# Kernel optimization log

Hardware: AMD Instinct MI355X
Metric: run time of the kernel (lower is better)

## Reference

```python
import jax, jax.numpy as jnp
from jax import lax
import numpy as np

B = 65536


def setup_inputs() -> dict:
    key = jax.random.key(0)
    ks = jax.random.split(key, 7)
    return {
        "x": jax.random.normal(ks[0], (B, 1, 28, 28), dtype=jnp.float32),
        "W1": jax.random.normal(ks[1], (8, 1, 3, 3), dtype=jnp.float32) * 0.3,
        "b1": jax.random.normal(ks[2], (8,), dtype=jnp.float32) * 0.1,
        "W2": jax.random.normal(ks[3], (16, 8, 3, 3), dtype=jnp.float32) * 0.1,
        "b2": jax.random.normal(ks[4], (16,), dtype=jnp.float32) * 0.1,
        "Wfc": jax.random.normal(ks[5], (1, 784), dtype=jnp.float32) * 0.03,
        "bfc": jax.random.normal(ks[6], (1,), dtype=jnp.float32) * 0.1,
    }


def _conv(x, w, b):
    # NCHW / OIHW, stride 2, padding 1 (matches nn.Conv2d(kernel=3, stride=2, padding=1))
    y = lax.conv_general_dilated(x, w, window_strides=(2, 2), padding=((1, 1), (1, 1)))
    return y + b[None, :, None, None]


def reference(x, W1, b1, W2, b2, Wfc, bfc):
    z = jax.nn.relu(_conv(x, W1, b1))            # [B,8,14,14]
    z = jax.nn.relu(_conv(z, W2, b2))            # [B,16,7,7]
    z = z.reshape(z.shape[0], -1)                # [B,784], channel-major like torch flatten
    rates = jax.nn.softplus(z @ Wfc.T + bfc) + 0.001   # [B,1]
    rates = rates[:, 0]                          # [B]
    # Logistic ODE du/dt = -k*u, u(0)=1 over t in [0,1] -> u(1) = exp(-k)
    probs = 1.0 - jnp.exp(-rates)
    return jnp.clip(probs, 1e-6, 1.0 - 1e-6)
```

## Files before the change

### kernel.cpp

```cpp
#include <hip/hip_runtime.h>
#include <math.h>


typedef short bf16x8 __attribute__((ext_vector_type(8)));
typedef float f32x4  __attribute__((ext_vector_type(4)));

#define NBLOCKS 4096
#define Z1_RS 19
#define Z1_SLOTS (15 * Z1_RS)

static __device__ __forceinline__ short f2bf(float f) {
    union { float f; unsigned u; } v; v.f = f;
    unsigned r = v.u + 0x7FFF + ((v.u >> 16) & 1);
    return (short)(r >> 16);
}

__global__ __launch_bounds__(256, 4) void fused_cnn_mfma(
    const float* __restrict__ x,
    const float* __restrict__ W1, const float* __restrict__ b1,
    const float* __restrict__ W2, const float* __restrict__ b2,
    const float* __restrict__ Wfc, const float* __restrict__ bfc,
    float* __restrict__ out, int nimg)
{
    __shared__ float  simg[4][30 * 31];
    __shared__ bf16x8 sz1[4][Z1_SLOTS];

    const int tid  = threadIdx.x;
    const int w    = tid >> 6;
    const int lane = tid & 63;
    const int hi   = lane >> 4;
    const int lo   = lane & 15;

    for (int i = tid; i < 4 * 30 * 31; i += 256) ((float*)simg)[i] = 0.f;
    {
        bf16x8 zz = {0,0,0,0,0,0,0,0};
        for (int i = tid; i < 4 * Z1_SLOTS; i += 256) ((bf16x8*)sz1)[i] = zz;
    }

    bf16x8 wb[3];
    #pragma unroll
    for (int kk = 0; kk < 3; kk++) {
        const int tap = kk * 4 + hi;
        #pragma unroll
        for (int j = 0; j < 8; j++)
            wb[kk][j] = (tap < 9) ? f2bf(W2[lo * 72 + j * 9 + tap])
                                  : (short)0;
    }

    int posoff[4];
    #pragma unroll
    for (int t = 0; t < 4; t++) {
        int p = t * 16 + lo; if (p > 48) p = 48;
        int qy = p / 7, qx = p - qy * 7;
        posoff[t] = ((2 * qy) * Z1_RS + 2 * qx) * 16;
    }
    int tapoff[3];
    #pragma unroll
    for (int kk = 0; kk < 3; kk++) {
        int tap = kk * 4 + hi;
        int ty = tap / 3, tx = tap - ty * 3;
        tapoff[kk] = (tap < 9) ? (ty * Z1_RS + tx) * 16 : 0;
    }

    const float b2v = b2[lo];
    float wfc[4][4];
    #pragma unroll
    for (int t = 0; t < 4; t++)
        #pragma unroll
        for (int r = 0; r < 4; r++) {
            int p = t * 16 + hi * 4 + r;
            wfc[t][r] = (p < 49) ? Wfc[lo * 49 + p] : 0.f;
        }
    const float bfc0 = bfc[0];

    const int nquad = (nimg + 3) >> 2;
    const char* __restrict__ zb = (const char*)&sz1[w][0];

    for (int q = blockIdx.x; q < nquad; q += gridDim.x) {
        __syncthreads();

        {
            const float4* src = (const float4*)(x + (size_t)q * (4 * 784));
            for (int f = tid; f < 784; f += 256) {
                int im = f / 196, p4 = f - im * 196;
                if (q * 4 + im < nimg) {
                    float4 v = src[f];
                    int yy = p4 / 7, xx = (p4 - yy * 7) * 4;
                    float* d = &simg[im][(yy + 1) * 31 + xx + 1];
                    d[0] = v.x; d[1] = v.y; d[2] = v.z; d[3] = v.w;
                }
            }
        }
        __syncthreads();

        #pragma unroll
        for (int i = 0; i < 4; i++) {
            int p = i * 64 + lane;
            bool valid = (p < 196);
            int pc = valid ? p : 195;
            int py = pc / 14, px = pc - py * 14;
            const float* wbse = &simg[w][(2 * py) * 31 + 2 * px];
            float t0 = wbse[0],  t1 = wbse[1],  t2 = wbse[2];
            float t3 = wbse[31], t4 = wbse[32], t5 = wbse[33];
            float t6 = wbse[62], t7 = wbse[63], t8 = wbse[64];
            asm volatile("" : "+v"(t0), "+v"(t1), "+v"(t2), "+v"(t3), "+v"(t4),
                              "+v"(t5), "+v"(t6), "+v"(t7), "+v"(t8));
            bf16x8 zr;
            #pragma unroll
            for (int c = 0; c < 8; c += 2) {
                const float* wa = &W1[c * 9];
                const float* wc = &W1[(c + 1) * 9];
                float za = b1[c], zc = b1[c + 1];
                za = fmaf(t0, wa[0], za); zc = fmaf(t0, wc[0], zc);
                za = fmaf(t1, wa[1], za); zc = fmaf(t1, wc[1], zc);
                za = fmaf(t2, wa[2], za); zc = fmaf(t2, wc[2], zc);
                za = fmaf(t3, wa[3], za); zc = fmaf(t3, wc[3], zc);
                za = fmaf(t4, wa[4], za); zc = fmaf(t4, wc[4], zc);
                za = fmaf(t5, wa[5], za); zc = fmaf(t5, wc[5], zc);
                za = fmaf(t6, wa[6], za); zc = fmaf(t6, wc[6], zc);
                za = fmaf(t7, wa[7], za); zc = fmaf(t7, wc[7], zc);
                za = fmaf(t8, wa[8], za); zc = fmaf(t8, wc[8], zc);
                za = fmaxf(za, 0.f);      zc = fmaxf(zc, 0.f);
                zr[c]     = f2bf(za);
                zr[c + 1] = f2bf(zc);
            }
            if (valid) sz1[w][(py + 1) * Z1_RS + (px + 1)] = zr;
        }

        f32x4 acc[4];
        {
            f32x4 z4 = {0.f, 0.f, 0.f, 0.f};
            #pragma unroll
            for (int t = 0; t < 4; t++) acc[t] = z4;
        }
        #pragma unroll
        for (int t = 0; t < 4; t++) {
            #pragma unroll
            for (int kk = 0; kk < 3; kk++) {
                bf16x8 af = *(const bf16x8*)(zb + posoff[t] + tapoff[kk]);
                acc[t] = __builtin_amdgcn_mfma_f32_16x16x32_bf16(
                             af, wb[kk], acc[t], 0, 0, 0);
            }
        }

        float fc = 0.f;
        #pragma unroll
        for (int t = 0; t < 4; t++)
            #pragma unroll
            for (int r = 0; r < 4; r++) {
                float z = fmaxf(acc[t][r] + b2v, 0.f);
                fc = fmaf(z, wfc[t][r], fc);
            }
        #pragma unroll
        for (int off = 32; off > 0; off >>= 1)
            fc += __shfl_down(fc, off, 64);

        if (lane == 0) {
            int img = q * 4 + w;
            if (img < nimg) {
                float v    = fc + bfc0;
                float sp   = fmaxf(v, 0.f) + log1pf(expf(-fabsf(v)));
                float rate = sp + 0.001f;
                float pr   = 1.f - expf(-rate);
                out[img] = fminf(fmaxf(pr, 1e-6f), 1.f - 1e-6f);
            }
        }
    }
}

extern "C" void kernel_launch(void* const* d_in, const int* in_sizes, int n_in,
                              void* d_out, int out_size, void* d_ws, size_t ws_size,
                              hipStream_t stream) {
    const float* x   = (const float*)d_in[0];
    const float* W1  = (const float*)d_in[1];
    const float* b1  = (const float*)d_in[2];
    const float* W2  = (const float*)d_in[3];
    const float* b2  = (const float*)d_in[4];
    const float* Wfc = (const float*)d_in[5];
    const float* bfc = (const float*)d_in[6];
    float* out = (float*)d_out;

    const int nimg  = in_sizes[0] / 784;
    const int nquad = (nimg + 3) / 4;
    const int grid  = nquad < NBLOCKS ? nquad : NBLOCKS;

    fused_cnn_mfma<<<grid, 256, 0, stream>>>(x, W1, b1, W2, b2, Wfc, bfc,
                                             out, nimg);
}
```

Before: 356.0 us.

## Give each wave its own image, prefetch next input in registers, drop block barriers

Each wavefront now loads its own image straight into registers and keeps a register prefetch of the next image while it computes the current one. This removes both per-iteration __syncthreads. The shared image buffer is re-laid out with a 36-float row stride so it can be written with aligned float4 stores, and per-lane address offsets are precomputed outside the loop. The bf16 packing now uses the hardware v_cvt_pk_bf16_f32 instruction instead of software rounding, which raises register pressure in exchange for latency hiding.

```diff
diff --git a/kernel.cpp b/kernel.cpp
--- a/kernel.cpp
+++ b/kernel.cpp
@@ -8,6 +8,9 @@
 #define NBLOCKS 4096
 #define Z1_RS 19
 #define Z1_SLOTS (15 * Z1_RS)
+#define IMG_RS 36
+#define IMG_ROWS 29
+#define IMG_FLOATS (IMG_ROWS * IMG_RS)
 
 static __device__ __forceinline__ short f2bf(float f) {
     union { float f; unsigned u; } v; v.f = f;
@@ -22,7 +25,7 @@
     const float* __restrict__ Wfc, const float* __restrict__ bfc,
     float* __restrict__ out, int nimg)
 {
-    __shared__ float  simg[4][30 * 31];
+    __shared__ __align__(16) float simg[4][IMG_FLOATS];
     __shared__ bf16x8 sz1[4][Z1_SLOTS];
 
     const int tid  = threadIdx.x;
@@ -31,10 +34,12 @@
     const int hi   = lane >> 4;
     const int lo   = lane & 15;
 
-    for (int i = tid; i < 4 * 30 * 31; i += 256) ((float*)simg)[i] = 0.f;
     {
+        f32x4 z4 = {0.f, 0.f, 0.f, 0.f};
+        f32x4* sp = (f32x4*)&simg[w][0];
+        for (int i = lane; i < IMG_FLOATS / 4; i += 64) sp[i] = z4;
         bf16x8 zz = {0,0,0,0,0,0,0,0};
-        for (int i = tid; i < 4 * Z1_SLOTS; i += 256) ((bf16x8*)sz1)[i] = zz;
+        for (int i = lane; i < Z1_SLOTS; i += 64) sz1[w][i] = zz;
     }
 
     bf16x8 wb[3];
@@ -62,6 +67,24 @@
         tapoff[kk] = (tap < 9) ? (ty * Z1_RS + tx) * 16 : 0;
     }
 
+    int src4[4], dstf[4];
+    #pragma unroll
+    for (int j = 0; j < 4; j++) {
+        int p4 = j * 64 + lane; if (p4 > 195) p4 = 195;
+        int yy = p4 / 7, xq = p4 - yy * 7;
+        src4[j] = p4;
+        dstf[j] = (yy + 1) * IMG_RS + 4 + 4 * xq;
+    }
+
+    int wboff[4], zoff[4];
+    #pragma unroll
+    for (int i = 0; i < 4; i++) {
+        int p = i * 64 + lane; if (p > 195) p = 195;
+        int py = p / 14, px = p - py * 14;
+        wboff[i] = (2 * py) * IMG_RS + 2 * px + 3;
+        zoff[i]  = ((py + 1) * Z1_RS + px + 1) * 16;
+    }
+
     const float b2v = b2[lo];
     float wfc[4][4];
     #pragma unroll
@@ -74,38 +97,44 @@
     const float bfc0 = bfc[0];
 
     const int nquad = (nimg + 3) >> 2;
-    const char* __restrict__ zb = (const char*)&sz1[w][0];
+    float* const sw = &simg[w][0];
+    char* const z1b = (char*)&sz1[w][0];
+
+    float4 pf[4];
+    {
+        int img = blockIdx.x * 4 + w;
+        if (img >= nimg) img = nimg - 1;
+        const float4* sp = (const float4*)(x + (size_t)img * 784);
+        #pragma unroll
+        for (int j = 0; j < 4; j++) pf[j] = sp[src4[j]];
+    }
 
     for (int q = blockIdx.x; q < nquad; q += gridDim.x) {
-        __syncthreads();
+        *(float4*)(sw + dstf[0]) = pf[0];
+        *(float4*)(sw + dstf[1]) = pf[1];
+        *(float4*)(sw + dstf[2]) = pf[2];
+        if (lane < 4) *(float4*)(sw + dstf[3]) = pf[3];
 
         {
-            const float4* src = (const float4*)(x + (size_t)q * (4 * 784));
-            for (int f = tid; f < 784; f += 256) {
-                int im = f / 196, p4 = f - im * 196;
-                if (q * 4 + im < nimg) {
-                    float4 v = src[f];
-                    int yy = p4 / 7, xx = (p4 - yy * 7) * 4;
-                    float* d = &simg[im][(yy + 1) * 31 + xx + 1];
-                    d[0] = v.x; d[1] = v.y; d[2] = v.z; d[3] = v.w;
-                }
-            }
-        }
-        __syncthreads();
+            int qn = q + gridDim.x;
+            if (qn < nquad) {
+                int imgn = qn * 4 + w;
+                if (imgn >= nimg) imgn = nimg - 1;
+                const float4* sp = (const float4*)(x + (size_t)imgn * 784);
+                #pragma unroll
+                for (int j = 0; j < 4; j++) pf[j] = sp[src4[j]];
+            }
+        }
 
         #pragma unroll
         for (int i = 0; i < 4; i++) {
-            int p = i * 64 + lane;
-            bool valid = (p < 196);
-            int pc = valid ? p : 195;
-            int py = pc / 14, px = pc - py * 14;
-            const float* wbse = &simg[w][(2 * py) * 31 + 2 * px];
-            float t0 = wbse[0],  t1 = wbse[1],  t2 = wbse[2];
-            float t3 = wbse[31], t4 = wbse[32], t5 = wbse[33];
-            float t6 = wbse[62], t7 = wbse[63], t8 = wbse[64];
+            const float* wbse = sw + wboff[i];
+            float t0 = wbse[0],            t1 = wbse[1],            t2 = wbse[2];
+            float t3 = wbse[IMG_RS],       t4 = wbse[IMG_RS + 1],   t5 = wbse[IMG_RS + 2];
+            float t6 = wbse[2 * IMG_RS],   t7 = wbse[2 * IMG_RS + 1], t8 = wbse[2 * IMG_RS + 2];
             asm volatile("" : "+v"(t0), "+v"(t1), "+v"(t2), "+v"(t3), "+v"(t4),
                               "+v"(t5), "+v"(t6), "+v"(t7), "+v"(t8));
-            bf16x8 zr;
+            union { bf16x8 v; unsigned u[4]; } zz;
             #pragma unroll
             for (int c = 0; c < 8; c += 2) {
                 const float* wa = &W1[c * 9];
@@ -121,10 +150,11 @@
                 za = fmaf(t7, wa[7], za); zc = fmaf(t7, wc[7], zc);
                 za = fmaf(t8, wa[8], za); zc = fmaf(t8, wc[8], zc);
                 za = fmaxf(za, 0.f);      zc = fmaxf(zc, 0.f);
-                zr[c]     = f2bf(za);
-                zr[c + 1] = f2bf(zc);
-            }
-            if (valid) sz1[w][(py + 1) * Z1_RS + (px + 1)] = zr;
+                unsigned pk;
+                asm("v_cvt_pk_bf16_f32 %0, %1, %2" : "=v"(pk) : "v"(za), "v"(zc));
+                zz.u[c >> 1] = pk;
+            }
+            if (i < 3 || lane < 4) *(bf16x8*)(z1b + zoff[i]) = zz.v;
         }
 
         f32x4 acc[4];
@@ -137,7 +167,7 @@
         for (int t = 0; t < 4; t++) {
             #pragma unroll
             for (int kk = 0; kk < 3; kk++) {
-                bf16x8 af = *(const bf16x8*)(zb + posoff[t] + tapoff[kk]);
+                bf16x8 af = *(const bf16x8*)(z1b + posoff[t] + tapoff[kk]);
                 acc[t] = __builtin_amdgcn_mfma_f32_16x16x32_bf16(
                              af, wb[kk], acc[t], 0, 0, 0);
             }
```

After: 358.0 us. Within noise of the previous version (+0.6%).
